# Kernel optimization log

Hardware: AMD Instinct MI355X
Metric: run time of the kernel (lower is better)

Reference implementation:

```python
import jax, jax.numpy as jnp
import numpy as np

TEMP = 0.2
L_MAIN, L_VIEW, L_SUP, L_UNSUP = 1.0, 1.0, 1.0, 0.2
N, D, V, P, NEG, U = 100000, 256, 3, 1024, 1024, 2048


def setup_inputs() -> dict:
    key = jax.random.key(0)
    ks = jax.random.split(key, 8)
    fused_logit = jax.random.normal(ks[0], (N,), dtype=jnp.float32)
    view_logits = jax.random.normal(ks[1], (V, N), dtype=jnp.float32)
    proj = jax.random.normal(ks[2], (V, N, D), dtype=jnp.float32)
    proj = proj / jnp.linalg.norm(proj, axis=-1, keepdims=True)  # 'already normalized'
    labels = jax.random.randint(ks[3], (N,), 0, 2).astype(jnp.float32)
    train_mask = jax.random.randint(ks[4], (N,), 0, 2).astype(bool)
    train_pos_idx = jax.random.randint(ks[5], (P,), 0, N)
    train_neg_idx = jax.random.randint(ks[6], (NEG,), 0, N)
    unlabeled_idx = jax.random.randint(ks[7], (U,), 0, N)  # len == max_unsup_samples -> no subsampling
    return dict(fused_logit=fused_logit, view_logits=view_logits, proj=proj,
                labels=labels, train_mask=train_mask, train_pos_idx=train_pos_idx,
                train_neg_idx=train_neg_idx, unlabeled_idx=unlabeled_idx)


def _masked_bce(logits, labels, mask):
    # BCEWithLogitsLoss mean over masked elements (stable formulation)
    bce = jnp.maximum(logits, 0) - logits * labels + jnp.log1p(jnp.exp(-jnp.abs(logits)))
    mf = mask.astype(logits.dtype)
    return jnp.sum(bce * mf) / jnp.maximum(jnp.sum(mf), 1.0)


def _sup_contrastive(proj, pos_idx, neg_idx, temp):
    lab_idx = jnp.concatenate([pos_idx, neg_idx])
    node_labels = jnp.concatenate([jnp.ones(pos_idx.shape[0]), jnp.zeros(neg_idx.shape[0])])
    L = lab_idx.shape[0]
    Vv = proj.shape[0]
    z = proj[:, lab_idx, :].transpose(1, 0, 2)          # [L, V, D]
    zf = z.reshape(L * Vv, -1)                           # [L*V, D]
    sim = (zf @ zf.T) / temp                             # [L*V, L*V]
    sim = sim - jax.lax.stop_gradient(sim.max(axis=1, keepdims=True))
    es = jnp.exp(sim)
    node = jnp.repeat(jnp.arange(L), Vv)
    view = jnp.tile(jnp.arange(Vv), L)
    flab = jnp.repeat(node_labels, Vv)
    sn = node[:, None] == node[None, :]
    sv = view[:, None] == view[None, :]
    sl = flab[:, None] == flab[None, :]
    eye = jnp.eye(L * Vv, dtype=bool)
    pos_m = ((sn & ~sv) | (~sn & sl)) & ~eye
    neg_m = (~sn) & (~sl) & ~eye
    den_m = pos_m | neg_m
    denom = jnp.sum(es * den_m.astype(es.dtype), axis=1) + 1e-12
    posf = pos_m.astype(es.dtype)
    log_prob = -jnp.log((es * posf + 1e-12) / denom[:, None])
    pos_count = pos_m.sum(axis=1)
    loss_per_anchor = jnp.sum(log_prob * posf, axis=1) / (pos_count.astype(es.dtype) + 1e-12)
    valid = ((pos_count > 0) & (den_m.sum(axis=1) > 0)).astype(es.dtype)
    return jnp.sum(loss_per_anchor * valid) / jnp.maximum(jnp.sum(valid), 1.0)


def _unsup_consistency(proj, unl_idx, temp):
    # Vectorized form of the double python loop: full cosine-sim matrix with
    # masked denominator (all but self) and positives = same node, other views.
    Vv = proj.shape[0]
    z = proj[:, unl_idx, :].transpose(1, 0, 2)           # [U, V, D]
    Uu = z.shape[0]
    M = Uu * Vv
    zf = z.reshape(M, -1)
    zn = zf / (jnp.linalg.norm(zf, axis=1, keepdims=True) + 1e-8)
    es = jnp.exp((zn @ zn.T) / temp)                     # [M, M]
    denom = es.sum(axis=1) - jnp.diag(es) + 1e-12        # exclude self
    node = jnp.repeat(jnp.arange(Uu), Vv)
    view = jnp.tile(jnp.arange(Vv), Uu)
    pos_m = (node[:, None] == node[None, :]) & (view[:, None] != view[None, :])
    posf = pos_m.astype(es.dtype)
    log_prob = -jnp.log(es / denom[:, None])
    per_anchor = jnp.sum(log_prob * posf, axis=1) / (Vv - 1)
    return jnp.mean(per_anchor)


def reference(fused_logit, view_logits, proj, labels, train_mask,
              train_pos_idx, train_neg_idx, unlabeled_idx):
    main_loss = _masked_bce(fused_logit, labels, train_mask)
    view_loss = jnp.mean(jax.vmap(lambda lg: _masked_bce(lg, labels, train_mask))(view_logits))
    sup_loss = _sup_contrastive(proj, train_pos_idx, train_neg_idx, TEMP)
    unsup_loss = _unsup_consistency(proj, unlabeled_idx, TEMP)
    total = L_MAIN * main_loss + L_VIEW * view_loss + L_SUP * sup_loss + L_UNSUP * unsup_loss
    return jnp.stack([total, main_loss, view_loss, sup_loss, unsup_loss])
```

## Files before the change

kernel.cpp:

```cpp
#include <hip/hip_runtime.h>
#include <math.h>

typedef short short8 __attribute__((ext_vector_type(8)));
typedef float floatx4 __attribute__((ext_vector_type(4)));

#define TEMP_INV 5.0f
#define W_UNSUP 0.2f
#define NB_BCE 256

static __device__ __forceinline__ unsigned short f2bf(float f) {
  unsigned int u = __float_as_uint(f);
  u += 0x7FFFu + ((u >> 16) & 1u);
  return (unsigned short)(u >> 16);
}

__device__ __forceinline__ float block_sum256(float v) {
  __shared__ float sh[4];
  for (int m = 1; m <= 32; m <<= 1) v += __shfl_xor(v, m);
  __syncthreads();
  if ((threadIdx.x & 63) == 0) sh[threadIdx.x >> 6] = v;
  __syncthreads();
  return sh[0] + sh[1] + sh[2] + sh[3];
}

__global__ void detect_kernel(const unsigned int* __restrict__ w, int nw, int* __restrict__ flag) {
  __shared__ int s_int, s_flt;
  if (threadIdx.x == 0) { s_int = 1; s_flt = 1; }
  __syncthreads();
  for (int i = threadIdx.x; i < nw; i += blockDim.x) {
    unsigned int x = w[i];
    if (x != 0u && x != 1u) s_int = 0;
    if (x != 0u && x != 0x3F800000u) s_flt = 0;
  }
  __syncthreads();
  if (threadIdx.x == 0) *flag = s_int ? 0 : (s_flt ? 1 : 2);
}

__global__ __launch_bounds__(256) void bce_kernel(
    const float* __restrict__ fused, const float* __restrict__ viewl,
    const float* __restrict__ labels, const void* __restrict__ maskp,
    const int* __restrict__ flagp, float* __restrict__ partials, int N, int V) {
  const int flag = *flagp;
  float cnt = 0.f, sm = 0.f;
  float sv[8];
  for (int v = 0; v < 8; v++) sv[v] = 0.f;
  const int Vc = V > 8 ? 8 : V;
  for (int i = blockIdx.x * blockDim.x + threadIdx.x; i < N; i += gridDim.x * blockDim.x) {
    bool m;
    if (flag == 0)      m = ((const int*)maskp)[i] != 0;
    else if (flag == 1) m = ((const float*)maskp)[i] != 0.0f;
    else                m = ((const unsigned char*)maskp)[i] != 0;
    if (!m) continue;
    float y = labels[i];
    cnt += 1.0f;
    float x = fused[i];
    sm += fmaxf(x, 0.f) - x * y + log1pf(__expf(-fabsf(x)));
    for (int v = 0; v < Vc; v++) {
      float xv = viewl[(size_t)v * N + i];
      sv[v] += fmaxf(xv, 0.f) - xv * y + log1pf(__expf(-fabsf(xv)));
    }
  }
  float tot = block_sum256(cnt);
  if (threadIdx.x == 0) partials[blockIdx.x * 16 + 0] = tot;
  tot = block_sum256(sm);
  if (threadIdx.x == 0) partials[blockIdx.x * 16 + 1] = tot;
  for (int v = 0; v < Vc; v++) {
    tot = block_sum256(sv[v]);
    if (threadIdx.x == 0) partials[blockIdx.x * 16 + 2 + v] = tot;
  }
}

__global__ __launch_bounds__(256) void gather_kernel(
    const float* __restrict__ proj, const int* __restrict__ pos_idx,
    const int* __restrict__ neg_idx, const int* __restrict__ unl_idx,
    unsigned short* __restrict__ zsup, unsigned short* __restrict__ zuns,
    float* __restrict__ dsup, float* __restrict__ duns,
    float* __restrict__ Esup, float* __restrict__ Bsup,
    float* __restrict__ Euns, float* __restrict__ Buns,
    int N, int D, int V, int P, int Msup, int Muns) {
  const int prob = blockIdx.y;
  const int M = prob ? Muns : Msup;
  const int r0 = blockIdx.x * 8;
  const int t = threadIdx.x;
  if (t < 8) {
    int rz = r0 + t;
    if (rz < M) {
      if (prob) { Euns[rz] = 0.f; Buns[rz] = 0.f; }
      else      { Esup[rz] = 0.f; Bsup[rz] = 0.f; }
    }
  }
  const int sub = t >> 5, ln = t & 31;
  const int r = r0 + sub;
  if (r >= M) return;
  const int l = r / V, v = r - l * V;
  const int idx = prob ? unl_idx[l] : (l < P ? pos_idx[l] : neg_idx[l - P]);
  const float* src = proj + ((size_t)v * N + (size_t)idx) * D + ln * 8;
  floatx4 p0 = *(const floatx4*)(src);
  floatx4 p1 = *(const floatx4*)(src + 4);
  float s = 0.f;
#pragma unroll
  for (int k = 0; k < 4; k++) s += p0[k] * p0[k] + p1[k] * p1[k];
  for (int m = 1; m <= 16; m <<= 1) s += __shfl_xor(s, m);
  const float n2 = s;
  float sc = 1.0f, dval = n2 * TEMP_INV;
  if (prob) {
    sc = 1.0f / (sqrtf(n2) + 1e-8f);
    dval = n2 * sc * sc * TEMP_INV;
  }
  short8 vv;
#pragma unroll
  for (int k = 0; k < 4; k++) {
    vv[k]     = (short)f2bf(p0[k] * sc);
    vv[k + 4] = (short)f2bf(p1[k] * sc);
  }
  unsigned short* zd = prob ? zuns : zsup;
  *(short8*)(zd + (size_t)r * 256 + ln * 8) = vv;
  if (ln == 0) (prob ? duns : dsup)[r] = dval;
}

__global__ __launch_bounds__(256) void sim_kernel(
    const unsigned short* __restrict__ zsup, const unsigned short* __restrict__ zuns,
    float* __restrict__ Esup, float* __restrict__ Bsup,
    float* __restrict__ Euns, float* __restrict__ Buns,
    int Msup, int Muns, int PV, int V,
    int Tsup, int Tuns, int nsSup, int nsUns) {
  const int prob = blockIdx.y;
  const unsigned short* __restrict__ z = prob ? zuns : zsup;
  float* __restrict__ Ep = prob ? Euns : Esup;
  float* __restrict__ Bp = prob ? Buns : Bsup;
  const int M = prob ? Muns : Msup;
  const int ns = prob ? nsUns : nsSup;
  const int T = prob ? Tuns : Tsup;
  const int t = blockIdx.x;
  if (t >= T) return;

#define TRI_BASE(s) ((s) * ns - ((s) * ((s) - 1)) / 2)
  int si = (int)((2.0f * ns + 1.0f -
                  sqrtf((2.0f * ns + 1.0f) * (2.0f * ns + 1.0f) - 8.0f * (float)t)) * 0.5f);
  if (si < 0) si = 0;
  if (si > ns - 1) si = ns - 1;
  while (si > 0 && TRI_BASE(si) > t) si--;
  while (si < ns - 1 && TRI_BASE(si + 1) <= t) si++;
  const int sj = si + (t - TRI_BASE(si));
#undef TRI_BASE

  const int R0 = si * 64, C0 = sj * 64;
  const int tid = threadIdx.x;
  const int wave = tid >> 6;
  const int wr = wave >> 1, wc = wave & 1;
  const int q = (tid >> 4) & 3;
  const int n16 = tid & 15;

  __shared__ __align__(16) unsigned short lds[64 * 264];
  __shared__ float redRE[64], redRB[64], redCE[64], redCB[64];

#pragma unroll
  for (int cc = 0; cc < 8; cc++) {
    int chunk = cc * 256 + tid;
    int rrow = chunk >> 5;
    int off = (chunk & 31) * 8;
    int gcol = C0 + rrow;
    short8 vv = {0, 0, 0, 0, 0, 0, 0, 0};
    if (gcol < M) vv = *(const short8*)(z + (size_t)gcol * 256 + off);
    *(short8*)(&lds[rrow * 264 + off]) = vv;
  }
  if (tid < 64) { redRE[tid] = 0.f; redRB[tid] = 0.f; redCE[tid] = 0.f; redCB[tid] = 0.f; }

  short8 a[2][8];
#pragma unroll
  for (int m = 0; m < 2; m++) {
    int row = R0 + wr * 32 + m * 16 + n16;
    if (row >= M) row = M - 1;
    const unsigned short* zr = z + (size_t)row * 256 + q * 8;
#pragma unroll
    for (int ks = 0; ks < 8; ks++) a[m][ks] = *(const short8*)(zr + ks * 32);
  }

  int bs[2][4], be[2][4];
#pragma unroll
  for (int m = 0; m < 2; m++)
#pragma unroll
    for (int r = 0; r < 4; r++) {
      int row = R0 + wr * 32 + m * 16 + q * 4 + r;
      if (row >= M) row = M - 1;
      if (prob == 0) { bs[m][r] = row < PV ? 0 : PV; be[m][r] = row < PV ? PV : M; }
      else           { int b0 = (row / V) * V; bs[m][r] = b0; be[m][r] = b0 + V; }
    }

  __syncthreads();

  floatx4 acc00 = {0.f, 0.f, 0.f, 0.f}, acc01 = {0.f, 0.f, 0.f, 0.f};
  floatx4 acc10 = {0.f, 0.f, 0.f, 0.f}, acc11 = {0.f, 0.f, 0.f, 0.f};
#pragma unroll
  for (int ks = 0; ks < 8; ks++) {
    const unsigned short* bp = &lds[(wc * 32 + n16) * 264 + q * 8 + ks * 32];
    short8 b0 = *(const short8*)bp;
    short8 b1 = *(const short8*)(bp + 16 * 264);
    acc00 = __builtin_amdgcn_mfma_f32_16x16x32_bf16(a[0][ks], b0, acc00, 0, 0, 0);
    acc01 = __builtin_amdgcn_mfma_f32_16x16x32_bf16(a[0][ks], b1, acc01, 0, 0, 0);
    acc10 = __builtin_amdgcn_mfma_f32_16x16x32_bf16(a[1][ks], b0, acc10, 0, 0, 0);
    acc11 = __builtin_amdgcn_mfma_f32_16x16x32_bf16(a[1][ks], b1, acc11, 0, 0, 0);
  }

  float er0[4] = {0, 0, 0, 0}, er1[4] = {0, 0, 0, 0};
  float br0[4] = {0, 0, 0, 0}, br1[4] = {0, 0, 0, 0};
  float ec0 = 0.f, ec1 = 0.f, bc0 = 0.f, bc1 = 0.f;
  const int j0 = C0 + wc * 32 + n16;
  const int j1 = j0 + 16;

#define EPI(ACC, MM, JN, ECOL, BCOL, ERA, BRA)                        \
  _Pragma("unroll")                                                   \
  for (int r = 0; r < 4; r++) {                                       \
    int row = R0 + wr * 32 + MM * 16 + q * 4 + r;                     \
    float tv = ACC[r] * TEMP_INV;                                     \
    bool valid = (row < M) && (JN < M);                               \
    float e = valid ? __expf(tv - 5.0f) : 0.0f;                       \
    float bv = (valid && JN >= bs[MM][r] && JN < be[MM][r]) ? tv : 0.0f; \
    ERA[r] += e; BRA[r] += bv; ECOL += e; BCOL += bv;                 \
  }
  EPI(acc00, 0, j0, ec0, bc0, er0, br0)
  EPI(acc01, 0, j1, ec1, bc1, er0, br0)
  EPI(acc10, 1, j0, ec0, bc0, er1, br1)
  EPI(acc11, 1, j1, ec1, bc1, er1, br1)
#undef EPI

#pragma unroll
  for (int mr = 0; mr < 8; mr++) {
    const int m = mr >> 2, r = mr & 3;
    float e = m ? er1[r] : er0[r];
    float b = m ? br1[r] : br0[r];
    for (int msk = 1; msk <= 8; msk <<= 1) { e += __shfl_xor(e, msk); b += __shfl_xor(b, msk); }
    if (n16 == 0) {
      int lr = wr * 32 + m * 16 + q * 4 + r;
      atomicAdd(&redRE[lr], e);
      atomicAdd(&redRB[lr], b);
    }
  }
  if (si != sj) {
    float e = ec0, b = bc0;
    e += __shfl_xor(e, 16); e += __shfl_xor(e, 32);
    b += __shfl_xor(b, 16); b += __shfl_xor(b, 32);
    if (q == 0) { atomicAdd(&redCE[wc * 32 + n16], e); atomicAdd(&redCB[wc * 32 + n16], b); }
    e = ec1; b = bc1;
    e += __shfl_xor(e, 16); e += __shfl_xor(e, 32);
    b += __shfl_xor(b, 16); b += __shfl_xor(b, 32);
    if (q == 0) { atomicAdd(&redCE[wc * 32 + 16 + n16], e); atomicAdd(&redCB[wc * 32 + 16 + n16], b); }
  }

  __syncthreads();
  if (tid < 64) {
    int row = R0 + tid;
    if (row < M) { atomicAdd(&Ep[row], redRE[tid]); atomicAdd(&Bp[row], redRB[tid]); }
    if (si != sj) {
      int col = C0 + tid;
      if (col < M) { atomicAdd(&Ep[col], redCE[tid]); atomicAdd(&Bp[col], redCB[tid]); }
    }
  }
}

__global__ __launch_bounds__(256) void finalize_kernel(
    const float* __restrict__ partials,
    const float* __restrict__ Esup, const float* __restrict__ Bsup, const float* __restrict__ dsup,
    const float* __restrict__ Euns, const float* __restrict__ Buns, const float* __restrict__ duns,
    int Msup, int Muns, int PV, int P, int NEG, int V, float* __restrict__ out) {
  const int t = threadIdx.x;
  float cnt = 0.f, sm = 0.f, sv[8];
  for (int v = 0; v < 8; v++) sv[v] = 0.f;
  const int Vc = V > 8 ? 8 : V;
  for (int b = t; b < NB_BCE; b += 256) {
    cnt += partials[b * 16 + 0];
    sm  += partials[b * 16 + 1];
    for (int v = 0; v < Vc; v++) sv[v] += partials[b * 16 + 2 + v];
  }
  cnt = block_sum256(cnt);
  sm = block_sum256(sm);
  float svt = 0.f;
  for (int v = 0; v < Vc; v++) svt += block_sum256(sv[v]);
  const float denomC = fmaxf(cnt, 1.0f);
  const float main_loss = sm / denomC;
  const float view_loss = (svt / denomC) / (float)V;

  float ssup = 0.f;
  for (int row = t; row < Msup; row += 256) {
    float E = Esup[row], B = Bsup[row];
    float d = dsup[row];
    float dn = E - __expf(d - 5.0f);
    float cl = (row < PV) ? (float)P : (float)NEG;
    float pc = (float)(V - 1) + (cl - 1.0f) * (float)V;
    ssup += logf(dn) + 5.0f - (B - d) / pc;
  }
  ssup = block_sum256(ssup);
  const float sup_loss = ssup / (float)Msup;

  float suns = 0.f;
  for (int row = t; row < Muns; row += 256) {
    float E = Euns[row], B = Buns[row];
    float d = duns[row];
    float dn = E - __expf(d - 5.0f);
    suns += logf(dn) + 5.0f - (B - d) / (float)(V - 1);
  }
  suns = block_sum256(suns);
  const float unsup_loss = suns / (float)Muns;

  if (t == 0) {
    float total = main_loss + view_loss + sup_loss + W_UNSUP * unsup_loss;
    out[0] = total;
    out[1] = main_loss;
    out[2] = view_loss;
    out[3] = sup_loss;
    out[4] = unsup_loss;
  }
}

extern "C" void kernel_launch(void* const* d_in, const int* in_sizes, int n_in,
                              void* d_out, int out_size, void* d_ws, size_t ws_size,
                              hipStream_t stream) {
  const float* fused  = (const float*)d_in[0];
  const float* viewl  = (const float*)d_in[1];
  const float* proj   = (const float*)d_in[2];
  const float* labels = (const float*)d_in[3];
  const void*  maskp  = d_in[4];
  const int* pos_idx  = (const int*)d_in[5];
  const int* neg_idx  = (const int*)d_in[6];
  const int* unl_idx  = (const int*)d_in[7];

  const int N = in_sizes[0];
  const int V = in_sizes[1] / N;
  const int D = in_sizes[2] / in_sizes[1];
  const int P = in_sizes[5];
  const int NEG = in_sizes[6];
  const int U = in_sizes[7];
  const int L = P + NEG;
  const int Msup = L * V;
  const int Muns = U * V;
  const int PV = P * V;

  char* ws = (char*)d_ws;
  size_t off = 0;
  auto alloc = [&](size_t bytes) { size_t o = off; off += (bytes + 255) & ~(size_t)255; return o; };
  const size_t o_flag = alloc(4);
  const size_t o_part = alloc((size_t)NB_BCE * 16 * 4);
  const size_t o_zsup = alloc((size_t)Msup * D * 2);
  const size_t o_zuns = alloc((size_t)Muns * D * 2);
  const size_t o_dsup = alloc((size_t)Msup * 4);
  const size_t o_duns = alloc((size_t)Muns * 4);
  const size_t o_Esup = alloc((size_t)Msup * 4);
  const size_t o_Bsup = alloc((size_t)Msup * 4);
  const size_t o_Euns = alloc((size_t)Muns * 4);
  const size_t o_Buns = alloc((size_t)Muns * 4);

  int* flag = (int*)(ws + o_flag);
  float* partials = (float*)(ws + o_part);
  unsigned short* zsup = (unsigned short*)(ws + o_zsup);
  unsigned short* zuns = (unsigned short*)(ws + o_zuns);
  float* dsup = (float*)(ws + o_dsup);
  float* duns = (float*)(ws + o_duns);
  float* Esup = (float*)(ws + o_Esup);
  float* Bsup = (float*)(ws + o_Bsup);
  float* Euns = (float*)(ws + o_Euns);
  float* Buns = (float*)(ws + o_Buns);

  int nw = N / 4 < 256 ? N / 4 : 256;
  detect_kernel<<<1, 256, 0, stream>>>((const unsigned int*)maskp, nw, flag);
  bce_kernel<<<NB_BCE, 256, 0, stream>>>(fused, viewl, labels, maskp, flag, partials, N, V);

  const int Mmax = Msup > Muns ? Msup : Muns;
  dim3 ggrid((Mmax + 7) / 8, 2);
  gather_kernel<<<ggrid, 256, 0, stream>>>(proj, pos_idx, neg_idx, unl_idx,
                                           zsup, zuns, dsup, duns,
                                           Esup, Bsup, Euns, Buns,
                                           N, D, V, P, Msup, Muns);

  const int nsS = (Msup + 63) / 64;
  const int nsU = (Muns + 63) / 64;
  const int Ts = nsS * (nsS + 1) / 2;
  const int Tu = nsU * (nsU + 1) / 2;
  const int Tmax = Ts > Tu ? Ts : Tu;
  dim3 sgrid(Tmax, 2);
  sim_kernel<<<sgrid, 256, 0, stream>>>(zsup, zuns, Esup, Bsup, Euns, Buns,
                                        Msup, Muns, PV, V, Ts, Tu, nsS, nsU);

  finalize_kernel<<<1, 256, 0, stream>>>(partials, Esup, Bsup, dsup, Euns, Buns, duns,
                                         Msup, Muns, PV, P, NEG, V, (float*)d_out);
}
```

Baseline: 496.6 us.

## Make sim kernel persistent over row strips with strided column tiles

Replaces the one-block-per-triangular-tile grid with blocks that each own a 64-row strip and loop over column tiles strided by NSPLIT. The A fragments stay in registers across iterations, and row sums build up in registers before a single atomic flush per row. This removes per-tile A reloads, the triangular index decode and the shared-memory reduction stage. In exchange it cuts the number of blocks, leaves work uneven across strips, and pushes column sums straight to global atomics.

```diff
diff --git a/kernel.cpp b/kernel.cpp
--- a/kernel.cpp
+++ b/kernel.cpp
@@ -7,6 +7,7 @@
 #define TEMP_INV 5.0f
 #define W_UNSUP 0.2f
 #define NB_BCE 256
+#define NSPLIT 8
 
 static __device__ __forceinline__ unsigned short f2bf(float f) {
   unsigned int u = __float_as_uint(f);
@@ -122,29 +123,19 @@
     const unsigned short* __restrict__ zsup, const unsigned short* __restrict__ zuns,
     float* __restrict__ Esup, float* __restrict__ Bsup,
     float* __restrict__ Euns, float* __restrict__ Buns,
-    int Msup, int Muns, int PV, int V,
-    int Tsup, int Tuns, int nsSup, int nsUns) {
+    int Msup, int Muns, int PV, int V, int nsSup, int nsUns) {
   const int prob = blockIdx.y;
   const unsigned short* __restrict__ z = prob ? zuns : zsup;
   float* __restrict__ Ep = prob ? Euns : Esup;
   float* __restrict__ Bp = prob ? Buns : Bsup;
   const int M = prob ? Muns : Msup;
   const int ns = prob ? nsUns : nsSup;
-  const int T = prob ? Tuns : Tsup;
-  const int t = blockIdx.x;
-  if (t >= T) return;
-
-#define TRI_BASE(s) ((s) * ns - ((s) * ((s) - 1)) / 2)
-  int si = (int)((2.0f * ns + 1.0f -
-                  sqrtf((2.0f * ns + 1.0f) * (2.0f * ns + 1.0f) - 8.0f * (float)t)) * 0.5f);
-  if (si < 0) si = 0;
-  if (si > ns - 1) si = ns - 1;
-  while (si > 0 && TRI_BASE(si) > t) si--;
-  while (si < ns - 1 && TRI_BASE(si + 1) <= t) si++;
-  const int sj = si + (t - TRI_BASE(si));
-#undef TRI_BASE
-
-  const int R0 = si * 64, C0 = sj * 64;
+
+  const int si = blockIdx.x / NSPLIT;
+  const int s  = blockIdx.x - si * NSPLIT;
+  if (si >= ns) return;
+
+  const int R0 = si * 64;
   const int tid = threadIdx.x;
   const int wave = tid >> 6;
   const int wr = wave >> 1, wc = wave & 1;
@@ -152,19 +143,6 @@
   const int n16 = tid & 15;
 
   __shared__ __align__(16) unsigned short lds[64 * 264];
-  __shared__ float redRE[64], redRB[64], redCE[64], redCB[64];
-
-#pragma unroll
-  for (int cc = 0; cc < 8; cc++) {
-    int chunk = cc * 256 + tid;
-    int rrow = chunk >> 5;
-    int off = (chunk & 31) * 8;
-    int gcol = C0 + rrow;
-    short8 vv = {0, 0, 0, 0, 0, 0, 0, 0};
-    if (gcol < M) vv = *(const short8*)(z + (size_t)gcol * 256 + off);
-    *(short8*)(&lds[rrow * 264 + off]) = vv;
-  }
-  if (tid < 64) { redRE[tid] = 0.f; redRB[tid] = 0.f; redCE[tid] = 0.f; redCB[tid] = 0.f; }
 
   short8 a[2][8];
 #pragma unroll
@@ -187,26 +165,40 @@
       else           { int b0 = (row / V) * V; bs[m][r] = b0; be[m][r] = b0 + V; }
     }
 
-  __syncthreads();
-
-  floatx4 acc00 = {0.f, 0.f, 0.f, 0.f}, acc01 = {0.f, 0.f, 0.f, 0.f};
-  floatx4 acc10 = {0.f, 0.f, 0.f, 0.f}, acc11 = {0.f, 0.f, 0.f, 0.f};
-#pragma unroll
-  for (int ks = 0; ks < 8; ks++) {
-    const unsigned short* bp = &lds[(wc * 32 + n16) * 264 + q * 8 + ks * 32];
-    short8 b0 = *(const short8*)bp;
-    short8 b1 = *(const short8*)(bp + 16 * 264);
-    acc00 = __builtin_amdgcn_mfma_f32_16x16x32_bf16(a[0][ks], b0, acc00, 0, 0, 0);
-    acc01 = __builtin_amdgcn_mfma_f32_16x16x32_bf16(a[0][ks], b1, acc01, 0, 0, 0);
-    acc10 = __builtin_amdgcn_mfma_f32_16x16x32_bf16(a[1][ks], b0, acc10, 0, 0, 0);
-    acc11 = __builtin_amdgcn_mfma_f32_16x16x32_bf16(a[1][ks], b1, acc11, 0, 0, 0);
-  }
-
   float er0[4] = {0, 0, 0, 0}, er1[4] = {0, 0, 0, 0};
   float br0[4] = {0, 0, 0, 0}, br1[4] = {0, 0, 0, 0};
-  float ec0 = 0.f, ec1 = 0.f, bc0 = 0.f, bc1 = 0.f;
-  const int j0 = C0 + wc * 32 + n16;
-  const int j1 = j0 + 16;
+
+  for (int tj = si + s; tj < ns; tj += NSPLIT) {
+    const int C0 = tj * 64;
+    __syncthreads();
+#pragma unroll
+    for (int cc = 0; cc < 8; cc++) {
+      int chunk = cc * 256 + tid;
+      int rrow = chunk >> 5;
+      int off = (chunk & 31) * 8;
+      int gcol = C0 + rrow;
+      short8 vv = {0, 0, 0, 0, 0, 0, 0, 0};
+      if (gcol < M) vv = *(const short8*)(z + (size_t)gcol * 256 + off);
+      *(short8*)(&lds[rrow * 264 + off]) = vv;
+    }
+    __syncthreads();
+
+    floatx4 acc00 = {0.f, 0.f, 0.f, 0.f}, acc01 = {0.f, 0.f, 0.f, 0.f};
+    floatx4 acc10 = {0.f, 0.f, 0.f, 0.f}, acc11 = {0.f, 0.f, 0.f, 0.f};
+#pragma unroll
+    for (int ks = 0; ks < 8; ks++) {
+      const unsigned short* bp = &lds[(wc * 32 + n16) * 264 + q * 8 + ks * 32];
+      short8 b0 = *(const short8*)bp;
+      short8 b1 = *(const short8*)(bp + 16 * 264);
+      acc00 = __builtin_amdgcn_mfma_f32_16x16x32_bf16(a[0][ks], b0, acc00, 0, 0, 0);
+      acc01 = __builtin_amdgcn_mfma_f32_16x16x32_bf16(a[0][ks], b1, acc01, 0, 0, 0);
+      acc10 = __builtin_amdgcn_mfma_f32_16x16x32_bf16(a[1][ks], b0, acc10, 0, 0, 0);
+      acc11 = __builtin_amdgcn_mfma_f32_16x16x32_bf16(a[1][ks], b1, acc11, 0, 0, 0);
+    }
+
+    float ec0 = 0.f, ec1 = 0.f, bc0 = 0.f, bc1 = 0.f;
+    const int j0 = C0 + wc * 32 + n16;
+    const int j1 = j0 + 16;
 
 #define EPI(ACC, MM, JN, ECOL, BCOL, ERA, BRA)                        \
   _Pragma("unroll")                                                   \
@@ -218,11 +210,23 @@
     float bv = (valid && JN >= bs[MM][r] && JN < be[MM][r]) ? tv : 0.0f; \
     ERA[r] += e; BRA[r] += bv; ECOL += e; BCOL += bv;                 \
   }
-  EPI(acc00, 0, j0, ec0, bc0, er0, br0)
-  EPI(acc01, 0, j1, ec1, bc1, er0, br0)
-  EPI(acc10, 1, j0, ec0, bc0, er1, br1)
-  EPI(acc11, 1, j1, ec1, bc1, er1, br1)
+    EPI(acc00, 0, j0, ec0, bc0, er0, br0)
+    EPI(acc01, 0, j1, ec1, bc1, er0, br0)
+    EPI(acc10, 1, j0, ec0, bc0, er1, br1)
+    EPI(acc11, 1, j1, ec1, bc1, er1, br1)
 #undef EPI
+
+    if (tj != si) {
+      float e = ec0, b = bc0;
+      e += __shfl_xor(e, 16); e += __shfl_xor(e, 32);
+      b += __shfl_xor(b, 16); b += __shfl_xor(b, 32);
+      if (q == 0 && j0 < M) { atomicAdd(&Ep[j0], e); atomicAdd(&Bp[j0], b); }
+      e = ec1; b = bc1;
+      e += __shfl_xor(e, 16); e += __shfl_xor(e, 32);
+      b += __shfl_xor(b, 16); b += __shfl_xor(b, 32);
+      if (q == 0 && j1 < M) { atomicAdd(&Ep[j1], e); atomicAdd(&Bp[j1], b); }
+    }
+  }
 
 #pragma unroll
   for (int mr = 0; mr < 8; mr++) {
@@ -230,30 +234,10 @@
     float e = m ? er1[r] : er0[r];
     float b = m ? br1[r] : br0[r];
     for (int msk = 1; msk <= 8; msk <<= 1) { e += __shfl_xor(e, msk); b += __shfl_xor(b, msk); }
-    if (n16 == 0) {
-      int lr = wr * 32 + m * 16 + q * 4 + r;
-      atomicAdd(&redRE[lr], e);
-      atomicAdd(&redRB[lr], b);
-    }
-  }
-  if (si != sj) {
-    float e = ec0, b = bc0;
-    e += __shfl_xor(e, 16); e += __shfl_xor(e, 32);
-    b += __shfl_xor(b, 16); b += __shfl_xor(b, 32);
-    if (q == 0) { atomicAdd(&redCE[wc * 32 + n16], e); atomicAdd(&redCB[wc * 32 + n16], b); }
-    e = ec1; b = bc1;
-    e += __shfl_xor(e, 16); e += __shfl_xor(e, 32);
-    b += __shfl_xor(b, 16); b += __shfl_xor(b, 32);
-    if (q == 0) { atomicAdd(&redCE[wc * 32 + 16 + n16], e); atomicAdd(&redCB[wc * 32 + 16 + n16], b); }
-  }
-
-  __syncthreads();
-  if (tid < 64) {
-    int row = R0 + tid;
-    if (row < M) { atomicAdd(&Ep[row], redRE[tid]); atomicAdd(&Bp[row], redRB[tid]); }
-    if (si != sj) {
-      int col = C0 + tid;
-      if (col < M) { atomicAdd(&Ep[col], redCE[tid]); atomicAdd(&Bp[col], redCB[tid]); }
+    int row = R0 + wr * 32 + m * 16 + q * 4 + r;
+    if (n16 == 0 && row < M) {
+      atomicAdd(&Ep[row], e);
+      atomicAdd(&Bp[row], b);
     }
   }
 }
@@ -373,12 +357,10 @@
 
   const int nsS = (Msup + 63) / 64;
   const int nsU = (Muns + 63) / 64;
-  const int Ts = nsS * (nsS + 1) / 2;
-  const int Tu = nsU * (nsU + 1) / 2;
-  const int Tmax = Ts > Tu ? Ts : Tu;
-  dim3 sgrid(Tmax, 2);
+  const int nsMax = nsS > nsU ? nsS : nsU;
+  dim3 sgrid(nsMax * NSPLIT, 2);
   sim_kernel<<<sgrid, 256, 0, stream>>>(zsup, zuns, Esup, Bsup, Euns, Buns,
-                                        Msup, Muns, PV, V, Ts, Tu, nsS, nsU);
+                                        Msup, Muns, PV, V, nsS, nsU);
 
   finalize_kernel<<<1, 256, 0, stream>>>(partials, Esup, Bsup, dsup, Euns, Buns, duns,
                                          Msup, Muns, PV, P, NEG, V, (float*)d_out);
```

Result: faster. 463.4 us (-6.7%).
